# Optimization experiments

Measured on AMD Instinct MI355X. Metric: run time of the kernel, lower is better.

The kernel has to match this reference:

```python
import jax, jax.numpy as jnp
import numpy as np

R = 32  # reduced channel dim = outplane // reduction
TRI_I, TRI_J = np.triu_indices(R)  # static upper-triangle indices (528 pairs)


def setup_inputs() -> dict:
    key = jax.random.key(0)
    k1, k2, k3 = jax.random.split(key, 3)
    B, Cin, H, W = 8, 256, 96, 96
    Cout = 256
    tri = R * (R + 1) // 2  # 528
    x = jax.random.normal(k1, (B, Cin, H, W), dtype=jnp.float32)
    # 1x1 conv weights stored as [out, in] matrices
    w_reduce = jax.random.normal(k2, (R, Cin), dtype=jnp.float32) * (1.0 / np.sqrt(Cin))
    w_recover = jax.random.normal(k3, (Cout, tri), dtype=jnp.float32) * (1.0 / np.sqrt(tri))
    return {"x": x, "w_reduce": w_reduce, "w_recover": w_recover}


def reference(x, w_reduce, w_recover):
    # reduce: 1x1 conv (no bias): [B,Cin,H,W] -> [B,R,H,W]
    out = jnp.einsum('bchw,rc->brhw', x, w_reduce)
    # per-pixel outer product, but only the upper-triangle entries:
    # bilinear[b,i,j,h,w] = out[b,i,h,w] * out[b,j,h,w]; gather (i,j) in triu
    i = jnp.asarray(TRI_I)
    j = jnp.asarray(TRI_J)
    up = out[:, i, :, :] * out[:, j, :, :]  # [B, 528, H, W]
    # channelRecover: 1x1 conv 528 -> Cout
    y = jnp.einsum('bthw,ot->bohw', up, w_recover)
    # signed sqrt
    return jnp.sign(y) * jnp.sqrt(jnp.abs(y) + 1e-6)
```

## Files before the change

### kernel.cpp

```cpp
#include <hip/hip_runtime.h>
#include <hip/hip_bf16.h>
#include <math.h>

#define HW     9216
#define CIN    256
#define RCH    32
#define NTRI   528
#define COUT   256
#define NB     8
#define WFROWS 272
#define UPROW  300

typedef _Float16 f16x8 __attribute__((ext_vector_type(8)));
typedef _Float16 f16x4 __attribute__((ext_vector_type(4)));
typedef float    f32x4 __attribute__((ext_vector_type(4)));

struct TriTab { unsigned char i[544]; unsigned char j[544]; };
constexpr TriTab make_tri() {
  TriTab t{};
  int ii = 0, jj = 0;
  for (int k = 0; k < 544; ++k) {
    if (k < NTRI) {
      t.i[k] = (unsigned char)ii; t.j[k] = (unsigned char)jj;
      if (++jj == 32) { ++ii; jj = ii; }
    } else { t.i[k] = 0; t.j[k] = 0; }
  }
  return t;
}
constexpr TriTab TRI = make_tri();

template<int TQ, int HALF>
__device__ __forceinline__ void build_up(const float (&o)[RCH], _Float16* rowp) {
  constexpr int NG  = HALF ? 8 : 9;
  constexpr int TLB = TQ * (HALF ? 32 : 36);
  constexpr int TB  = HALF ? 288 : 0;
#pragma unroll
  for (int g = 0; g < NG; ++g) {
    f16x4 v;
#pragma unroll
    for (int s = 0; s < 4; ++s) {
      const int tl = TLB + g * 4 + s;
      const int t  = TB + tl;
      float f = (t < NTRI) ? o[TRI.i[t]] * o[TRI.j[t]] : 0.0f;
      v[s] = (_Float16)f;
    }
    *(f16x4*)&rowp[TLB + g * 4] = v;
  }
}

template<int HALF>
__device__ __forceinline__ void build_dispatch(int wv, const float (&o)[RCH],
                                               _Float16* rowp) {
  switch (wv) {
    case 0: build_up<0, HALF>(o, rowp); break;
    case 1: build_up<1, HALF>(o, rowp); break;
    case 2: build_up<2, HALF>(o, rowp); break;
    case 3: build_up<3, HALF>(o, rowp); break;
    case 4: build_up<4, HALF>(o, rowp); break;
    case 5: build_up<5, HALF>(o, rowp); break;
    case 6: build_up<6, HALF>(o, rowp); break;
    default: build_up<7, HALF>(o, rowp); break;
  }
}

__global__ __launch_bounds__(256) void convert_kernel(
    const float* __restrict__ w_reduce, const float* __restrict__ w_recover,
    _Float16* __restrict__ w16, _Float16* __restrict__ wr16h,
    _Float16* __restrict__ wr16l) {
  const int bx = blockIdx.x;
  const int tid = threadIdx.x;
  if (bx < WFROWS) {
    const int wv  = bx / 34;
    const int rem = bx - wv * 34;
    const int mi  = rem / 17;
    const int c   = rem - mi * 17;
    const int lane = tid >> 2;
    const int s0   = (tid & 3) * 2;
    const int o = wv * 32 + mi * 16 + (lane & 15);
    const int t = c * 32 + (lane >> 4) * 8 + s0;
    float f0 = (t     < NTRI) ? w_recover[(size_t)o * NTRI + t]     : 0.0f;
    float f1 = (t + 1 < NTRI) ? w_recover[(size_t)o * NTRI + t + 1] : 0.0f;
    _Float16* p = &w16[((size_t)bx * 64 + lane) * 8 + s0];
    p[0] = (_Float16)f0;
    p[1] = (_Float16)f1;
  } else {
    int e = (bx - WFROWS) * 512 + tid;
#pragma unroll
    for (int k = 0; k < 2; ++k, e += 256) {
      float f = w_reduce[e];
      _Float16 h = (_Float16)f;
      wr16h[e] = h;
      wr16l[e] = (_Float16)(f - (float)h);
    }
  }
}

__global__ __launch_bounds__(256) void reduce_kernel(
    const float* __restrict__ x, const _Float16* __restrict__ wr16h,
    const _Float16* __restrict__ wr16l, float* __restrict__ out) {
  const int tid  = threadIdx.x;
  const int bx   = blockIdx.x;
  const int b    = bx / 144;
  const int p0   = (bx - b * 144) * 64;
  const int wv   = tid >> 6;
  const int lane = tid & 63;
  const int ml   = lane & 15;
  const int q    = lane >> 4;

  f32x4 acc[2];
#pragma unroll
  for (int mt = 0; mt < 2; ++mt)
#pragma unroll
    for (int r2 = 0; r2 < 4; ++r2) acc[mt][r2] = 0.0f;

  const float* xb = x + (size_t)b * CIN * HW + p0 + wv * 16 + ml;

  float xv[2][8];
#pragma unroll
  for (int s = 0; s < 8; ++s)
    xv[0][s] = xb[(size_t)(q * 8 + s) * HW];

#pragma unroll
  for (int ch = 0; ch < 8; ++ch) {
    const int cur = ch & 1, nxt = cur ^ 1;
    if (ch < 7) {
#pragma unroll
      for (int s = 0; s < 8; ++s)
        xv[nxt][s] = xb[(size_t)((ch + 1) * 32 + q * 8 + s) * HW];
    }
    f16x8 xh, xl;
#pragma unroll
    for (int s = 0; s < 8; ++s) {
      float f = xv[cur][s];
      _Float16 h = (_Float16)f;
      xh[s] = h;
      xl[s] = (_Float16)(f - (float)h);
    }
#pragma unroll
    for (int mt = 0; mt < 2; ++mt) {
      const int off = (mt * 16 + ml) * CIN + ch * 32 + q * 8;
      f16x8 wh = *(const f16x8*)&wr16h[off];
      f16x8 wl = *(const f16x8*)&wr16l[off];
      acc[mt] = __builtin_amdgcn_mfma_f32_16x16x32_f16(wh, xh, acc[mt], 0, 0, 0);
      acc[mt] = __builtin_amdgcn_mfma_f32_16x16x32_f16(wl, xh, acc[mt], 0, 0, 0);
      acc[mt] = __builtin_amdgcn_mfma_f32_16x16x32_f16(wh, xl, acc[mt], 0, 0, 0);
    }
  }

#pragma unroll
  for (int mt = 0; mt < 2; ++mt)
#pragma unroll
    for (int reg = 0; reg < 4; ++reg)
      out[((size_t)(b * RCH + mt * 16 + q * 4 + reg)) * HW + p0 + wv * 16 + ml] =
          acc[mt][reg];
}

__global__ __launch_bounds__(512, 4) void gemm2_kernel(
    const float* __restrict__ outp, const _Float16* __restrict__ w16,
    float* __restrict__ y) {
  __shared__ __align__(16) _Float16 upS[64 * UPROW];

  const int tid  = threadIdx.x;
  const int bx   = blockIdx.x;
  const int b    = bx / 144;
  const int p0   = (bx - b * 144) * 64;
  const int wv   = tid >> 6;
  const int lane = tid & 63;
  const int ml   = lane & 15;
  const int q    = lane >> 4;

  const float* ob = outp + (size_t)b * RCH * HW + p0 + lane;
  float o0[RCH];
#pragma unroll
  for (int r = 0; r < RCH; ++r) o0[r] = ob[(size_t)r * HW];

  const _Float16* wf0 = w16 + ((size_t)(wv * 2 + 0) * 17 * 64 + lane) * 8;
  const _Float16* wf1 = w16 + ((size_t)(wv * 2 + 1) * 17 * 64 + lane) * 8;

  f16x8 abuf[3][2];
  abuf[0][0] = *(const f16x8*)&wf0[0];
  abuf[0][1] = *(const f16x8*)&wf1[0];
  abuf[1][0] = *(const f16x8*)&wf0[512];
  abuf[1][1] = *(const f16x8*)&wf1[512];

  f32x4 acc[2][4];
#pragma unroll
  for (int mi = 0; mi < 2; ++mi)
#pragma unroll
    for (int ni = 0; ni < 4; ++ni)
#pragma unroll
      for (int r2 = 0; r2 < 4; ++r2) acc[mi][ni][r2] = 0.0f;

  _Float16* rowp = &upS[lane * UPROW];

  build_dispatch<0>(wv, o0, rowp);
  __syncthreads();

  f16x8 bbuf[2][4];
#pragma unroll
  for (int ni = 0; ni < 4; ++ni)
    bbuf[0][ni] = *(const f16x8*)&upS[(ni * 16 + ml) * UPROW + q * 8];

#pragma unroll
  for (int c = 0; c < 9; ++c) {
    const int cur = c % 3;
    const int pf  = (c + 2) % 3;
    abuf[pf][0] = *(const f16x8*)&wf0[(size_t)(c + 2) * 512];
    abuf[pf][1] = *(const f16x8*)&wf1[(size_t)(c + 2) * 512];
    const int cb = c & 1, nb = cb ^ 1;
    if (c < 8) {
      const int t0n = (c + 1) * 32;
#pragma unroll
      for (int ni = 0; ni < 4; ++ni)
        bbuf[nb][ni] = *(const f16x8*)&upS[(ni * 16 + ml) * UPROW + t0n + q * 8];
    }
#pragma unroll
    for (int ni = 0; ni < 4; ++ni) {
      acc[0][ni] = __builtin_amdgcn_mfma_f32_16x16x32_f16(abuf[cur][0], bbuf[cb][ni], acc[0][ni], 0, 0, 0);
      acc[1][ni] = __builtin_amdgcn_mfma_f32_16x16x32_f16(abuf[cur][1], bbuf[cb][ni], acc[1][ni], 0, 0, 0);
    }
    __builtin_amdgcn_sched_group_barrier(0x020, 2, 0);
    if (c < 8)
      __builtin_amdgcn_sched_group_barrier(0x100, 4, 0);
    __builtin_amdgcn_sched_group_barrier(0x008, 8, 0);
  }

  float o1[RCH];
#pragma unroll
  for (int r = 0; r < RCH; ++r) o1[r] = ob[(size_t)r * HW];

  __syncthreads();

  build_dispatch<1>(wv, o1, rowp);
  __syncthreads();

#pragma unroll
  for (int ni = 0; ni < 4; ++ni)
    bbuf[0][ni] = *(const f16x8*)&upS[(ni * 16 + ml) * UPROW + q * 8];

#pragma unroll
  for (int cc = 0; cc < 8; ++cc) {
    const int cur = cc % 3;
    if (cc < 6) {
      const int pf = (2 + cc) % 3;
      abuf[pf][0] = *(const f16x8*)&wf0[(size_t)(11 + cc) * 512];
      abuf[pf][1] = *(const f16x8*)&wf1[(size_t)(11 + cc) * 512];
    }
    const int cb = cc & 1, nb = cb ^ 1;
    if (cc < 7) {
      const int t0n = (cc + 1) * 32;
#pragma unroll
      for (int ni = 0; ni < 4; ++ni)
        bbuf[nb][ni] = *(const f16x8*)&upS[(ni * 16 + ml) * UPROW + t0n + q * 8];
    }
#pragma unroll
    for (int ni = 0; ni < 4; ++ni) {
      acc[0][ni] = __builtin_amdgcn_mfma_f32_16x16x32_f16(abuf[cur][0], bbuf[cb][ni], acc[0][ni], 0, 0, 0);
      acc[1][ni] = __builtin_amdgcn_mfma_f32_16x16x32_f16(abuf[cur][1], bbuf[cb][ni], acc[1][ni], 0, 0, 0);
    }
    if (cc < 6)
      __builtin_amdgcn_sched_group_barrier(0x020, 2, 0);
    if (cc < 7)
      __builtin_amdgcn_sched_group_barrier(0x100, 4, 0);
    __builtin_amdgcn_sched_group_barrier(0x008, 8, 0);
  }

#pragma unroll
  for (int mi = 0; mi < 2; ++mi) {
#pragma unroll
    for (int reg = 0; reg < 4; ++reg) {
      const int o = wv * 32 + mi * 16 + q * 4 + reg;
      float* yrow = y + ((size_t)(b * COUT + o)) * HW + p0 + ml;
#pragma unroll
      for (int ni = 0; ni < 4; ++ni) {
        float v = acc[mi][ni][reg];
        float s = sqrtf(fabsf(v) + 1e-6f);
        yrow[ni * 16] = v > 0.0f ? s : (v < 0.0f ? -s : 0.0f);
      }
    }
  }
}

__global__ __launch_bounds__(512, 4) void fused_kernel(
    const float* __restrict__ x, const _Float16* __restrict__ w16,
    const _Float16* __restrict__ wr16h, const _Float16* __restrict__ wr16l,
    float* __restrict__ y) {
  __shared__ float outS[RCH * 68];
  __shared__ __align__(16) _Float16 upS[64 * UPROW];

  const int tid  = threadIdx.x;
  const int bx   = blockIdx.x;
  const int b    = bx / 144;
  const int p0   = (bx - b * 144) * 64;
  const int wv   = tid >> 6;
  const int lane = tid & 63;
  const int ml   = lane & 15;
  const int q    = lane >> 4;
  const int mt   = wv >> 2;
  const int nt   = wv & 3;

  {
    f32x4 g1acc;
#pragma unroll
    for (int r2 = 0; r2 < 4; ++r2) g1acc[r2] = 0.0f;

    const int abase = (mt * 16 + ml) * CIN + q * 8;
    f16x8 pa[3][2];
    pa[0][0] = *(const f16x8*)&wr16h[abase + 0 * 32];
    pa[0][1] = *(const f16x8*)&wr16l[abase + 0 * 32];
    pa[1][0] = *(const f16x8*)&wr16h[abase + 1 * 32];
    pa[1][1] = *(const f16x8*)&wr16l[abase + 1 * 32];

    const float* xb = x + (size_t)b * CIN * HW + p0 + nt * 16 + ml;
    float xv[64];
#pragma unroll
    for (int ch = 0; ch < 8; ++ch)
#pragma unroll
      for (int s = 0; s < 8; ++s)
        xv[ch * 8 + s] = xb[(size_t)(ch * 32 + q * 8 + s) * HW];
    __builtin_amdgcn_sched_barrier(0);

#pragma unroll
    for (int ch = 0; ch < 8; ++ch) {
      const int cur = ch % 3;
      if (ch + 2 < 8) {
        const int pf = (ch + 2) % 3;
        pa[pf][0] = *(const f16x8*)&wr16h[abase + (ch + 2) * 32];
        pa[pf][1] = *(const f16x8*)&wr16l[abase + (ch + 2) * 32];
      }
      f16x8 bh, bl;
#pragma unroll
      for (int s = 0; s < 8; ++s) {
        float f = xv[ch * 8 + s];
        _Float16 h = (_Float16)f;
        bh[s] = h;
        bl[s] = (_Float16)(f - (float)h);
      }
      g1acc = __builtin_amdgcn_mfma_f32_16x16x32_f16(pa[cur][0], bh, g1acc, 0, 0, 0);
      g1acc = __builtin_amdgcn_mfma_f32_16x16x32_f16(pa[cur][1], bh, g1acc, 0, 0, 0);
      g1acc = __builtin_amdgcn_mfma_f32_16x16x32_f16(pa[cur][0], bl, g1acc, 0, 0, 0);
    }
#pragma unroll
    for (int reg = 0; reg < 4; ++reg)
      outS[(mt * 16 + q * 4 + reg) * 68 + nt * 16 + ml] = g1acc[reg];
  }

  const _Float16* wf0 = w16 + ((size_t)(wv * 2 + 0) * 17 * 64 + lane) * 8;
  const _Float16* wf1 = w16 + ((size_t)(wv * 2 + 1) * 17 * 64 + lane) * 8;

  f16x8 abuf[3][2];
  abuf[0][0] = *(const f16x8*)&wf0[0];
  abuf[0][1] = *(const f16x8*)&wf1[0];
  abuf[1][0] = *(const f16x8*)&wf0[512];
  abuf[1][1] = *(const f16x8*)&wf1[512];

  __syncthreads();

  f32x4 acc[2][4];
#pragma unroll
  for (int mi = 0; mi < 2; ++mi)
#pragma unroll
    for (int ni = 0; ni < 4; ++ni)
#pragma unroll
      for (int r2 = 0; r2 < 4; ++r2) acc[mi][ni][r2] = 0.0f;

  _Float16* rowp = &upS[lane * UPROW];

  {
    float o[RCH];
#pragma unroll
    for (int r = 0; r < RCH; ++r) o[r] = outS[r * 68 + lane];
    build_dispatch<0>(wv, o, rowp);
  }
  __syncthreads();

  f16x8 bbuf[2][4];
#pragma unroll
  for (int ni = 0; ni < 4; ++ni)
    bbuf[0][ni] = *(const f16x8*)&upS[(ni * 16 + ml) * UPROW + q * 8];

#pragma unroll
  for (int c = 0; c < 9; ++c) {
    const int cur = c % 3;
    const int pf  = (c + 2) % 3;
    abuf[pf][0] = *(const f16x8*)&wf0[(size_t)(c + 2) * 512];
    abuf[pf][1] = *(const f16x8*)&wf1[(size_t)(c + 2) * 512];
    const int cb = c & 1, nb = cb ^ 1;
    if (c < 8) {
      const int t0n = (c + 1) * 32;
#pragma unroll
      for (int ni = 0; ni < 4; ++ni)
        bbuf[nb][ni] = *(const f16x8*)&upS[(ni * 16 + ml) * UPROW + t0n + q * 8];
    }
#pragma unroll
    for (int ni = 0; ni < 4; ++ni) {
      acc[0][ni] = __builtin_amdgcn_mfma_f32_16x16x32_f16(abuf[cur][0], bbuf[cb][ni], acc[0][ni], 0, 0, 0);
      acc[1][ni] = __builtin_amdgcn_mfma_f32_16x16x32_f16(abuf[cur][1], bbuf[cb][ni], acc[1][ni], 0, 0, 0);
    }
  }
  __syncthreads();

  {
    float o[RCH];
#pragma unroll
    for (int r = 0; r < RCH; ++r) o[r] = outS[r * 68 + lane];
    build_dispatch<1>(wv, o, rowp);
  }
  __syncthreads();

#pragma unroll
  for (int ni = 0; ni < 4; ++ni)
    bbuf[0][ni] = *(const f16x8*)&upS[(ni * 16 + ml) * UPROW + q * 8];

#pragma unroll
  for (int cc = 0; cc < 8; ++cc) {
    const int cur = cc % 3;
    if (cc < 6) {
      const int pf = (2 + cc) % 3;
      abuf[pf][0] = *(const f16x8*)&wf0[(size_t)(11 + cc) * 512];
      abuf[pf][1] = *(const f16x8*)&wf1[(size_t)(11 + cc) * 512];
    }
    const int cb = cc & 1, nb = cb ^ 1;
    if (cc < 7) {
      const int t0n = (cc + 1) * 32;
#pragma unroll
      for (int ni = 0; ni < 4; ++ni)
        bbuf[nb][ni] = *(const f16x8*)&upS[(ni * 16 + ml) * UPROW + t0n + q * 8];
    }
#pragma unroll
    for (int ni = 0; ni < 4; ++ni) {
      acc[0][ni] = __builtin_amdgcn_mfma_f32_16x16x32_f16(abuf[cur][0], bbuf[cb][ni], acc[0][ni], 0, 0, 0);
      acc[1][ni] = __builtin_amdgcn_mfma_f32_16x16x32_f16(abuf[cur][1], bbuf[cb][ni], acc[1][ni], 0, 0, 0);
    }
  }

#pragma unroll
  for (int mi = 0; mi < 2; ++mi) {
#pragma unroll
    for (int reg = 0; reg < 4; ++reg) {
      const int o = wv * 32 + mi * 16 + q * 4 + reg;
      float* yrow = y + ((size_t)(b * COUT + o)) * HW + p0 + ml;
#pragma unroll
      for (int ni = 0; ni < 4; ++ni) {
        float v = acc[mi][ni][reg];
        float s = sqrtf(fabsf(v) + 1e-6f);
        yrow[ni * 16] = v > 0.0f ? s : (v < 0.0f ? -s : 0.0f);
      }
    }
  }
}

extern "C" void kernel_launch(void* const* d_in, const int* in_sizes, int n_in,
                              void* d_out, int out_size, void* d_ws, size_t ws_size,
                              hipStream_t stream) {
  const float* x         = (const float*)d_in[0];
  const float* w_reduce  = (const float*)d_in[1];
  const float* w_recover = (const float*)d_in[2];
  float* y = (float*)d_out;

  _Float16* w16   = (_Float16*)d_ws;
  _Float16* wr16h = (_Float16*)((char*)d_ws + 278528);
  _Float16* wr16l = (_Float16*)((char*)d_ws + 278528 + 16384);
  float*    outp  = (float*)((char*)d_ws + 311296);
  const size_t NEED = 311296 + (size_t)NB * RCH * HW * 4;

  convert_kernel<<<WFROWS + 16, 256, 0, stream>>>(w_reduce, w_recover, w16, wr16h, wr16l);
  if (ws_size >= NEED) {
    reduce_kernel<<<NB * (HW / 64), 256, 0, stream>>>(x, wr16h, wr16l, outp);
    gemm2_kernel<<<NB * (HW / 64), 512, 0, stream>>>(outp, w16, y);
  } else {
    fused_kernel<<<NB * (HW / 64), 512, 0, stream>>>(x, w16, wr16h, wr16l, y);
  }
}
```

Baseline: 174.1 us.

## Replace split-fp16 MFMA reduce with fp32 FMA reduce using transposed LDS weights

The reduce 1x1 conv no longer splits x and weights into fp16 hi/lo pairs and runs three MFMAs per step. It now computes in plain fp32 FMAs: each thread owns one pixel and 32 accumulators. The convert kernel gains an extra block that writes a transposed fp32 copy of w_reduce, which each reduce block stages into shared memory and reads as broadcast vectors. Launch shape changes to 128-thread blocks covering 128 pixels, with double-buffered x loads. This drops the conversion and MFMA overhead on a memory-bound stage, at the cost of more scalar FMAs and fewer threads per block.

```diff
diff --git a/kernel.cpp b/kernel.cpp
--- a/kernel.cpp
+++ b/kernel.cpp
@@ -66,7 +66,7 @@
 __global__ __launch_bounds__(256) void convert_kernel(
     const float* __restrict__ w_reduce, const float* __restrict__ w_recover,
     _Float16* __restrict__ w16, _Float16* __restrict__ wr16h,
-    _Float16* __restrict__ wr16l) {
+    _Float16* __restrict__ wr16l, float* __restrict__ wT) {
   const int bx = blockIdx.x;
   const int tid = threadIdx.x;
   if (bx < WFROWS) {
@@ -83,7 +83,7 @@
     _Float16* p = &w16[((size_t)bx * 64 + lane) * 8 + s0];
     p[0] = (_Float16)f0;
     p[1] = (_Float16)f1;
-  } else {
+  } else if (bx < WFROWS + 16) {
     int e = (bx - WFROWS) * 512 + tid;
 #pragma unroll
     for (int k = 0; k < 2; ++k, e += 256) {
@@ -92,67 +92,71 @@
       wr16h[e] = h;
       wr16l[e] = (_Float16)(f - (float)h);
     }
-  }
-}
-
-__global__ __launch_bounds__(256) void reduce_kernel(
-    const float* __restrict__ x, const _Float16* __restrict__ wr16h,
-    const _Float16* __restrict__ wr16l, float* __restrict__ out) {
-  const int tid  = threadIdx.x;
-  const int bx   = blockIdx.x;
-  const int b    = bx / 144;
-  const int p0   = (bx - b * 144) * 64;
-  const int wv   = tid >> 6;
-  const int lane = tid & 63;
-  const int ml   = lane & 15;
-  const int q    = lane >> 4;
-
-  f32x4 acc[2];
-#pragma unroll
-  for (int mt = 0; mt < 2; ++mt)
-#pragma unroll
-    for (int r2 = 0; r2 < 4; ++r2) acc[mt][r2] = 0.0f;
-
-  const float* xb = x + (size_t)b * CIN * HW + p0 + wv * 16 + ml;
-
-  float xv[2][8];
-#pragma unroll
-  for (int s = 0; s < 8; ++s)
-    xv[0][s] = xb[(size_t)(q * 8 + s) * HW];
-
-#pragma unroll
-  for (int ch = 0; ch < 8; ++ch) {
-    const int cur = ch & 1, nxt = cur ^ 1;
-    if (ch < 7) {
-#pragma unroll
-      for (int s = 0; s < 8; ++s)
-        xv[nxt][s] = xb[(size_t)((ch + 1) * 32 + q * 8 + s) * HW];
-    }
-    f16x8 xh, xl;
-#pragma unroll
-    for (int s = 0; s < 8; ++s) {
-      float f = xv[cur][s];
-      _Float16 h = (_Float16)f;
-      xh[s] = h;
-      xl[s] = (_Float16)(f - (float)h);
-    }
-#pragma unroll
-    for (int mt = 0; mt < 2; ++mt) {
-      const int off = (mt * 16 + ml) * CIN + ch * 32 + q * 8;
-      f16x8 wh = *(const f16x8*)&wr16h[off];
-      f16x8 wl = *(const f16x8*)&wr16l[off];
-      acc[mt] = __builtin_amdgcn_mfma_f32_16x16x32_f16(wh, xh, acc[mt], 0, 0, 0);
-      acc[mt] = __builtin_amdgcn_mfma_f32_16x16x32_f16(wl, xh, acc[mt], 0, 0, 0);
-      acc[mt] = __builtin_amdgcn_mfma_f32_16x16x32_f16(wh, xl, acc[mt], 0, 0, 0);
-    }
-  }
-
-#pragma unroll
-  for (int mt = 0; mt < 2; ++mt)
-#pragma unroll
-    for (int reg = 0; reg < 4; ++reg)
-      out[((size_t)(b * RCH + mt * 16 + q * 4 + reg)) * HW + p0 + wv * 16 + ml] =
-          acc[mt][reg];
+  } else {
+#pragma unroll
+    for (int k = 0; k < 32; ++k) {
+      const int e = k * 256 + tid;
+      const int c = e >> 5;
+      const int r = e & 31;
+      wT[e] = w_reduce[r * CIN + c];
+    }
+  }
+}
+
+__global__ __launch_bounds__(128) void reduce_kernel(
+    const float* __restrict__ x, const float* __restrict__ wT,
+    float* __restrict__ out) {
+  __shared__ float wS[CIN * RCH];
+  const int tid = threadIdx.x;
+  const int bx  = blockIdx.x;
+  const int b   = bx / 72;
+  const int p0  = (bx - b * 72) * 128;
+
+#pragma unroll
+  for (int k = 0; k < 16; ++k) {
+    const int e = k * 512 + tid * 4;
+    *(f32x4*)&wS[e] = *(const f32x4*)&wT[e];
+  }
+  __syncthreads();
+
+  float acc[RCH];
+#pragma unroll
+  for (int r = 0; r < RCH; ++r) acc[r] = 0.0f;
+
+  const float* xb = x + (size_t)b * CIN * HW + p0 + tid;
+
+  float xv[2][16];
+#pragma unroll
+  for (int j = 0; j < 16; ++j)
+    xv[0][j] = xb[(size_t)j * HW];
+
+#pragma unroll
+  for (int g = 0; g < 16; ++g) {
+    const int cur = g & 1, nxt = cur ^ 1;
+    if (g < 15) {
+#pragma unroll
+      for (int j = 0; j < 16; ++j)
+        xv[nxt][j] = xb[(size_t)((g + 1) * 16 + j) * HW];
+      __builtin_amdgcn_sched_group_barrier(0x020, 16, 0);
+    }
+#pragma unroll
+    for (int j = 0; j < 16; ++j) {
+      const float xc = xv[cur][j];
+      const float* wrow = &wS[(g * 16 + j) * RCH];
+#pragma unroll
+      for (int r8 = 0; r8 < 8; ++r8) {
+        f32x4 w4 = *(const f32x4*)&wrow[r8 * 4];
+        acc[r8 * 4 + 0] += w4[0] * xc;
+        acc[r8 * 4 + 1] += w4[1] * xc;
+        acc[r8 * 4 + 2] += w4[2] * xc;
+        acc[r8 * 4 + 3] += w4[3] * xc;
+      }
+    }
+  }
+
+#pragma unroll
+  for (int r = 0; r < RCH; ++r)
+    out[((size_t)(b * RCH + r)) * HW + p0 + tid] = acc[r];
 }
 
 __global__ __launch_bounds__(512, 4) void gemm2_kernel(
@@ -461,12 +465,14 @@
   _Float16* w16   = (_Float16*)d_ws;
   _Float16* wr16h = (_Float16*)((char*)d_ws + 278528);
   _Float16* wr16l = (_Float16*)((char*)d_ws + 278528 + 16384);
-  float*    outp  = (float*)((char*)d_ws + 311296);
-  const size_t NEED = 311296 + (size_t)NB * RCH * HW * 4;
-
-  convert_kernel<<<WFROWS + 16, 256, 0, stream>>>(w_reduce, w_recover, w16, wr16h, wr16l);
+  float*    wT    = (float*)((char*)d_ws + 311296);
+  float*    outp  = (float*)((char*)d_ws + 344064);
+  const size_t NEED = 344064 + (size_t)NB * RCH * HW * 4;
+
+  convert_kernel<<<WFROWS + 17, 256, 0, stream>>>(w_reduce, w_recover, w16,
+                                                  wr16h, wr16l, wT);
   if (ws_size >= NEED) {
-    reduce_kernel<<<NB * (HW / 64), 256, 0, stream>>>(x, wr16h, wr16l, outp);
+    reduce_kernel<<<NB * (HW / 128), 128, 0, stream>>>(x, wT, outp);
     gemm2_kernel<<<NB * (HW / 64), 512, 0, stream>>>(outp, w16, y);
   } else {
     fused_kernel<<<NB * (HW / 64), 512, 0, stream>>>(x, w16, wr16h, wr16l, y);
```

Result: slower. 179.6 us (+3.1%).

## Stage x tiles through LDS with vectorized loads and double buffering in reduce kernel

Applied to the files above, without the earlier changes.

The reduce kernel now covers 128 pixels per block instead of 64. It loads x with coalesced float4 global loads into a double-buffered LDS tile, and each wave reads its MFMA B operands from LDS. This replaces the old strided scalar global loads and prefetches the next channel chunk and the weight fragments while the current MFMAs run. The change also adds an unused transposed copy of w_reduce (wT) to the convert kernel, which is extra work and extra workspace, and it halves the number of blocks in the reduce kernel.

```diff
diff --git a/kernel.cpp b/kernel.cpp
--- a/kernel.cpp
+++ b/kernel.cpp
@@ -10,10 +10,12 @@
 #define NB     8
 #define WFROWS 272
 #define UPROW  300
+#define PXW    130
 
 typedef _Float16 f16x8 __attribute__((ext_vector_type(8)));
 typedef _Float16 f16x4 __attribute__((ext_vector_type(4)));
 typedef float    f32x4 __attribute__((ext_vector_type(4)));
+typedef float    f32x2 __attribute__((ext_vector_type(2)));
 
 struct TriTab { unsigned char i[544]; unsigned char j[544]; };
 constexpr TriTab make_tri() {
@@ -66,7 +68,7 @@
 __global__ __launch_bounds__(256) void convert_kernel(
     const float* __restrict__ w_reduce, const float* __restrict__ w_recover,
     _Float16* __restrict__ w16, _Float16* __restrict__ wr16h,
-    _Float16* __restrict__ wr16l) {
+    _Float16* __restrict__ wr16l, float* __restrict__ wT) {
   const int bx = blockIdx.x;
   const int tid = threadIdx.x;
   if (bx < WFROWS) {
@@ -83,7 +85,7 @@
     _Float16* p = &w16[((size_t)bx * 64 + lane) * 8 + s0];
     p[0] = (_Float16)f0;
     p[1] = (_Float16)f1;
-  } else {
+  } else if (bx < WFROWS + 16) {
     int e = (bx - WFROWS) * 512 + tid;
 #pragma unroll
     for (int k = 0; k < 2; ++k, e += 256) {
@@ -92,67 +94,119 @@
       wr16h[e] = h;
       wr16l[e] = (_Float16)(f - (float)h);
     }
+  } else {
+#pragma unroll
+    for (int k = 0; k < 32; ++k) {
+      const int e = k * 256 + tid;
+      const int c = e >> 5;
+      const int r = e & 31;
+      wT[e] = w_reduce[r * CIN + c];
+    }
   }
 }
 
 __global__ __launch_bounds__(256) void reduce_kernel(
     const float* __restrict__ x, const _Float16* __restrict__ wr16h,
     const _Float16* __restrict__ wr16l, float* __restrict__ out) {
+  __shared__ __align__(16) float xS[2][RCH][PXW];
+
   const int tid  = threadIdx.x;
   const int bx   = blockIdx.x;
-  const int b    = bx / 144;
-  const int p0   = (bx - b * 144) * 64;
+  const int b    = bx / 72;
+  const int p0   = (bx - b * 72) * 128;
   const int wv   = tid >> 6;
   const int lane = tid & 63;
   const int ml   = lane & 15;
   const int q    = lane >> 4;
-
-  f32x4 acc[2];
+  const int ci   = tid >> 5;
+  const int pxi  = (tid & 31) * 4;
+
+  const float* xg = x + (size_t)b * CIN * HW + p0 + pxi;
+  const int arow0 = (0 * 16 + ml) * CIN + q * 8;
+  const int arow1 = (1 * 16 + ml) * CIN + q * 8;
+
+  f32x4 acc[2][2];
 #pragma unroll
   for (int mt = 0; mt < 2; ++mt)
 #pragma unroll
-    for (int r2 = 0; r2 < 4; ++r2) acc[mt][r2] = 0.0f;
-
-  const float* xb = x + (size_t)b * CIN * HW + p0 + wv * 16 + ml;
-
-  float xv[2][8];
-#pragma unroll
-  for (int s = 0; s < 8; ++s)
-    xv[0][s] = xb[(size_t)(q * 8 + s) * HW];
+    for (int nt = 0; nt < 2; ++nt)
+#pragma unroll
+      for (int r2 = 0; r2 < 4; ++r2) acc[mt][nt][r2] = 0.0f;
+
+  f32x4 gx[4];
+#pragma unroll
+  for (int k = 0; k < 4; ++k)
+    gx[k] = *(const f32x4*)&xg[(size_t)(ci + 8 * k) * HW];
+
+  f16x8 af[2][2][2];
+  af[0][0][0] = *(const f16x8*)&wr16h[arow0];
+  af[0][0][1] = *(const f16x8*)&wr16l[arow0];
+  af[0][1][0] = *(const f16x8*)&wr16h[arow1];
+  af[0][1][1] = *(const f16x8*)&wr16l[arow1];
+
+#pragma unroll
+  for (int k = 0; k < 4; ++k) {
+    *(f32x2*)&xS[0][ci + 8 * k][pxi]     = f32x2{gx[k][0], gx[k][1]};
+    *(f32x2*)&xS[0][ci + 8 * k][pxi + 2] = f32x2{gx[k][2], gx[k][3]};
+  }
+  __syncthreads();
 
 #pragma unroll
   for (int ch = 0; ch < 8; ++ch) {
     const int cur = ch & 1, nxt = cur ^ 1;
     if (ch < 7) {
-#pragma unroll
-      for (int s = 0; s < 8; ++s)
-        xv[nxt][s] = xb[(size_t)((ch + 1) * 32 + q * 8 + s) * HW];
-    }
-    f16x8 xh, xl;
-#pragma unroll
-    for (int s = 0; s < 8; ++s) {
-      float f = xv[cur][s];
-      _Float16 h = (_Float16)f;
-      xh[s] = h;
-      xl[s] = (_Float16)(f - (float)h);
-    }
-#pragma unroll
-    for (int mt = 0; mt < 2; ++mt) {
-      const int off = (mt * 16 + ml) * CIN + ch * 32 + q * 8;
-      f16x8 wh = *(const f16x8*)&wr16h[off];
-      f16x8 wl = *(const f16x8*)&wr16l[off];
-      acc[mt] = __builtin_amdgcn_mfma_f32_16x16x32_f16(wh, xh, acc[mt], 0, 0, 0);
-      acc[mt] = __builtin_amdgcn_mfma_f32_16x16x32_f16(wl, xh, acc[mt], 0, 0, 0);
-      acc[mt] = __builtin_amdgcn_mfma_f32_16x16x32_f16(wh, xl, acc[mt], 0, 0, 0);
+      const int c0n = (ch + 1) * 32;
+#pragma unroll
+      for (int k = 0; k < 4; ++k)
+        gx[k] = *(const f32x4*)&xg[(size_t)(c0n + ci + 8 * k) * HW];
+      af[nxt][0][0] = *(const f16x8*)&wr16h[arow0 + c0n];
+      af[nxt][0][1] = *(const f16x8*)&wr16l[arow0 + c0n];
+      af[nxt][1][0] = *(const f16x8*)&wr16h[arow1 + c0n];
+      af[nxt][1][1] = *(const f16x8*)&wr16l[arow1 + c0n];
+    }
+#pragma unroll
+    for (int nt = 0; nt < 2; ++nt) {
+      const int pxc = wv * 32 + nt * 16 + ml;
+      float bf[8];
+#pragma unroll
+      for (int s = 0; s < 8; ++s) bf[s] = xS[cur][q * 8 + s][pxc];
+      f16x8 bh, bl;
+#pragma unroll
+      for (int s = 0; s < 8; ++s) {
+        _Float16 h = (_Float16)bf[s];
+        bh[s] = h;
+        bl[s] = (_Float16)(bf[s] - (float)h);
+      }
+      acc[0][nt] = __builtin_amdgcn_mfma_f32_16x16x32_f16(af[cur][0][0], bh, acc[0][nt], 0, 0, 0);
+      acc[0][nt] = __builtin_amdgcn_mfma_f32_16x16x32_f16(af[cur][0][1], bh, acc[0][nt], 0, 0, 0);
+      acc[0][nt] = __builtin_amdgcn_mfma_f32_16x16x32_f16(af[cur][0][0], bl, acc[0][nt], 0, 0, 0);
+      acc[1][nt] = __builtin_amdgcn_mfma_f32_16x16x32_f16(af[cur][1][0], bh, acc[1][nt], 0, 0, 0);
+      acc[1][nt] = __builtin_amdgcn_mfma_f32_16x16x32_f16(af[cur][1][1], bh, acc[1][nt], 0, 0, 0);
+      acc[1][nt] = __builtin_amdgcn_mfma_f32_16x16x32_f16(af[cur][1][0], bl, acc[1][nt], 0, 0, 0);
+    }
+    if (ch < 7) {
+#pragma unroll
+      for (int k = 0; k < 4; ++k) {
+        *(f32x2*)&xS[nxt][ci + 8 * k][pxi]     = f32x2{gx[k][0], gx[k][1]};
+        *(f32x2*)&xS[nxt][ci + 8 * k][pxi + 2] = f32x2{gx[k][2], gx[k][3]};
+      }
+      __builtin_amdgcn_sched_group_barrier(0x020, 8, 0);
+      __builtin_amdgcn_sched_group_barrier(0x100, 16, 0);
+      __builtin_amdgcn_sched_group_barrier(0x002, 48, 0);
+      __builtin_amdgcn_sched_group_barrier(0x008, 12, 0);
+      __builtin_amdgcn_sched_group_barrier(0x200, 8, 0);
+      __syncthreads();
     }
   }
 
 #pragma unroll
   for (int mt = 0; mt < 2; ++mt)
 #pragma unroll
-    for (int reg = 0; reg < 4; ++reg)
-      out[((size_t)(b * RCH + mt * 16 + q * 4 + reg)) * HW + p0 + wv * 16 + ml] =
-          acc[mt][reg];
+    for (int nt = 0; nt < 2; ++nt)
+#pragma unroll
+      for (int reg = 0; reg < 4; ++reg)
+        out[((size_t)(b * RCH + mt * 16 + q * 4 + reg)) * HW + p0 + wv * 32 +
+            nt * 16 + ml] = acc[mt][nt][reg];
 }
 
 __global__ __launch_bounds__(512, 4) void gemm2_kernel(
@@ -461,12 +515,14 @@
   _Float16* w16   = (_Float16*)d_ws;
   _Float16* wr16h = (_Float16*)((char*)d_ws + 278528);
   _Float16* wr16l = (_Float16*)((char*)d_ws + 278528 + 16384);
-  float*    outp  = (float*)((char*)d_ws + 311296);
-  const size_t NEED = 311296 + (size_t)NB * RCH * HW * 4;
-
-  convert_kernel<<<WFROWS + 16, 256, 0, stream>>>(w_reduce, w_recover, w16, wr16h, wr16l);
+  float*    wT    = (float*)((char*)d_ws + 311296);
+  float*    outp  = (float*)((char*)d_ws + 344064);
+  const size_t NEED = 344064 + (size_t)NB * RCH * HW * 4;
+
+  convert_kernel<<<WFROWS + 17, 256, 0, stream>>>(w_reduce, w_recover, w16,
+                                                  wr16h, wr16l, wT);
   if (ws_size >= NEED) {
-    reduce_kernel<<<NB * (HW / 64), 256, 0, stream>>>(x, wr16h, wr16l, outp);
+    reduce_kernel<<<NB * (HW / 128), 256, 0, stream>>>(x, wr16h, wr16l, outp);
     gemm2_kernel<<<NB * (HW / 64), 512, 0, stream>>>(outp, w16, y);
   } else {
     fused_kernel<<<NB * (HW / 64), 512, 0, stream>>>(x, w16, wr16h, wr16l, y);
```

Result: faster. 168.2 us (-3.4%).
